# Optimization experiments

Hardware: AMD Instinct MI355X
Metric: run time of the kernel (lower is better)

Reference implementation:

```python
import jax, jax.numpy as jnp
import numpy as np

WS = 7  # window size

def rel_pos_index(ws):
    coords = np.stack(np.meshgrid(np.arange(ws), np.arange(ws), indexing='ij'))  # [2,ws,ws]
    cf = coords.reshape(2, -1)                      # [2, N]
    rel = (cf[:, :, None] - cf[:, None, :]).transpose(1, 2, 0)  # [N,N,2]
    rel[:, :, 0] += ws - 1
    rel[:, :, 1] += ws - 1
    rel[:, :, 0] *= 2 * ws - 1
    return rel.sum(-1)                              # [N,N] int

REL_IDX = rel_pos_index(WS)

def setup_inputs() -> dict:
    key = jax.random.key(0)
    ks = jax.random.split(key, 7)
    B, nW, H, N, D = 32, 64, 6, WS * WS, 32
    C = H * D
    return {
        "x": jax.random.normal(ks[0], (B * nW, N, C), jnp.float32),
        "q_global": jax.random.normal(ks[1], (B, 1, H, N, D), jnp.float32),
        "w_qkv": jax.random.normal(ks[2], (2 * C, C), jnp.float32) * 0.02,
        "b_qkv": jax.random.normal(ks[3], (2 * C,), jnp.float32) * 0.02,
        "bias_table": jax.random.normal(ks[4], ((2 * WS - 1) ** 2, H), jnp.float32) * 0.02,
        "w_proj": jax.random.normal(ks[5], (C, C), jnp.float32) * 0.02,
        "b_proj": jax.random.normal(ks[6], (C,), jnp.float32) * 0.02,
    }

def reference(x, q_global, w_qkv, b_qkv, bias_table, w_proj, b_proj):
    B_, N, C = x.shape
    B, _, H, _, D = q_global.shape
    scale = D ** -0.5
    # K,V projection: [B_, N, 2C] -> two [B_, H, N, D]
    kv = x @ w_qkv.T + b_qkv
    k, v = jnp.split(kv, 2, axis=-1)
    k = k.reshape(B_, N, H, D).transpose(0, 2, 1, 3)
    v = v.reshape(B_, N, H, D).transpose(0, 2, 1, 3)
    # Global query repeated over windows per image
    rep = B_ // B
    q = jnp.broadcast_to(q_global, (B, rep, H, N, D)).reshape(B_, H, N, D) * scale
    attn = jnp.einsum('bhnd,bhmd->bhnm', q, k)  # [B_, H, N, N]
    bias = bias_table[REL_IDX.reshape(-1)].reshape(N, N, H).transpose(2, 0, 1)  # [H,N,N]
    attn = jax.nn.softmax(attn + bias[None], axis=-1)
    out = jnp.einsum('bhnm,bhmd->bhnd', attn, v).transpose(0, 2, 1, 3).reshape(B_, N, C)
    return out @ w_proj.T + b_proj
```

## Files before the change

### kernel.cpp

```cpp
#include <hip/hip_runtime.h>
#include <hip/hip_bf16.h>

typedef __attribute__((ext_vector_type(8))) short short8;
typedef __attribute__((ext_vector_type(4))) short short4v;
typedef __attribute__((ext_vector_type(4))) float f32x4;

#define MFMA16(A,B,C) __builtin_amdgcn_mfma_f32_16x16x32_bf16((A),(B),(C),0,0,0)

static __device__ __forceinline__ unsigned short f2bf(float f) {
  unsigned int u = __float_as_uint(f);
  unsigned int rnd = 0x7fffu + ((u >> 16) & 1u);
  return (unsigned short)((u + rnd) >> 16);
}

__global__ void prep_kernel(const float* __restrict__ qg,
                            const float* __restrict__ wqkv,
                            const float* __restrict__ wproj,
                            const float* __restrict__ btab,
                            unsigned short* __restrict__ wq_c,
                            unsigned short* __restrict__ wp_c,
                            unsigned short* __restrict__ q_bf,
                            float* __restrict__ bias_c)
{
  const int t = blockIdx.x * 256 + threadIdx.x;
  if (t < 32*6*64*32) {
    const int d = t & 31, n = (t >> 5) & 63;
    const int bh = t >> 11;
    const int h = bh % 6, b = bh / 6;
    float v = 0.f;
    if (n < 49) v = qg[((b * 6 + h) * 49 + n) * 32 + d] * 0.17677669529663687f;
    q_bf[t] = f2bf(v);
  }
  if (t < 8*3*6*64*8) {
    const int e = t & 7, l = (t >> 3) & 63;
    const int kb = (t >> 9) % 6, g = (t >> 9) / 6;
    const int ct = g % 3, wv = g / 3;
    const int j = wv * 48 + ct * 16 + (l & 15);
    const int c = kb * 32 + (l >> 4) * 8 + e;
    wq_c[t] = f2bf(wqkv[j * 192 + c]);
  }
  if (t < 2*6*6*64*8) {
    const int e = t & 7, l = (t >> 3) & 63;
    const int kb = (t >> 9) % 6, g = (t >> 9) / 6;
    const int ct = g % 6, cc = g / 6;
    const int cp = cc * 96 + ct * 16 + (l & 15);
    const int c = kb * 32 + (l >> 4) * 8 + e;
    wp_c[t] = f2bf(wproj[cp * 192 + c]);
  }
  if (t < 6*4*64*16) {
    const int i4 = t & 15;
    const int mt = i4 >> 2, r = i4 & 3;
    const int l = (t >> 4) & 63;
    const int nt = (t >> 10) & 3;
    const int h = t >> 12;
    const int m = mt * 16 + (l >> 4) * 4 + r;
    const int n = nt * 16 + (l & 15);
    float v;
    if (m >= 49) v = -1e30f;
    else if (n >= 49) v = 0.f;
    else {
      const int ci = n / 7, cj = n % 7, mi = m / 7, mj = m % 7;
      const int idx = (ci - mi + 6) * 13 + (cj - mj + 6);
      v = btab[idx * 6 + h];
    }
    bias_c[t] = v;
  }
}

__global__ __launch_bounds__(512, 4)
void fused_win_attn(const float* __restrict__ x,
                    const float* __restrict__ b_qkv,
                    const float* __restrict__ b_proj,
                    const unsigned short* __restrict__ wq_c,
                    const unsigned short* __restrict__ wp_c,
                    const unsigned short* __restrict__ q_bf,
                    const float* __restrict__ bias_c,
                    float* __restrict__ out)
{
  extern __shared__ unsigned short lds[];
  unsigned short* x_lds  = lds;
  unsigned short* k_lds  = lds + 12800;
  unsigned short* vT_lds = lds + 26624;
  unsigned short* o_lds  = lds + 12800;

  const f32x4 ZERO4 = {0.f, 0.f, 0.f, 0.f};
  const int tid = threadIdx.x;
  const int wv = tid >> 6;
  const int l  = tid & 63;
  const int lr = l & 15;
  const int lq = l >> 4;
  const int w  = blockIdx.x;

  {
    const float* xw = x + (size_t)w * (49 * 192);
    for (int i = tid; i < 2352; i += 512) {
      const float4 v = *reinterpret_cast<const float4*>(xw + i * 4);
      const int e = i * 4;
      const int row = e / 192, col = e % 192;
      short4v pk;
      pk[0] = (short)f2bf(v.x); pk[1] = (short)f2bf(v.y);
      pk[2] = (short)f2bf(v.z); pk[3] = (short)f2bf(v.w);
      *reinterpret_cast<short4v*>(&x_lds[row * 200 + col]) = pk;
    }
    for (int i = tid; i < 720; i += 512) {
      const int e = i * 4;
      const int row = 49 + e / 192, col = e % 192;
      short4v z = {0, 0, 0, 0};
      *reinterpret_cast<short4v*>(&x_lds[row * 200 + col]) = z;
    }
  }
  __syncthreads();

  {
    short8 afr[4][6];
#pragma unroll
    for (int mt = 0; mt < 4; ++mt)
#pragma unroll
      for (int kb = 0; kb < 6; ++kb)
        afr[mt][kb] = *reinterpret_cast<const short8*>(
            &x_lds[(mt * 16 + lr) * 200 + kb * 32 + lq * 8]);

    for (int ct = 0; ct < 3; ++ct) {
      const int j = wv * 48 + ct * 16 + lr;
      short8 bfr[6];
#pragma unroll
      for (int kb = 0; kb < 6; ++kb)
        bfr[kb] = *reinterpret_cast<const short8*>(
            &wq_c[((((wv * 3) + ct) * 6 + kb) * 64 + l) * 8]);
      const float bq = b_qkv[j];
      f32x4 acc[4];
#pragma unroll
      for (int mt = 0; mt < 4; ++mt) acc[mt] = ZERO4;
#pragma unroll
      for (int kb = 0; kb < 6; ++kb)
#pragma unroll
        for (int mt = 0; mt < 4; ++mt)
          acc[mt] = MFMA16(afr[mt][kb], bfr[kb], acc[mt]);

      if (j < 192) {
        const int h = j >> 5, d = j & 31;
#pragma unroll
        for (int mt = 0; mt < 4; ++mt) {
          const int n0 = mt * 16 + lq * 4;
#pragma unroll
          for (int r = 0; r < 4; ++r)
            k_lds[h * 2304 + (n0 + r) * 36 + d] = f2bf(acc[mt][r] + bq);
        }
      } else {
        const int jj = j - 192, h = jj >> 5, d = jj & 31;
#pragma unroll
        for (int mt = 0; mt < 4; ++mt) {
          const int n0 = mt * 16 + lq * 4;
          short4v pk;
#pragma unroll
          for (int r = 0; r < 4; ++r) pk[r] = (short)f2bf(acc[mt][r] + bq);
          *reinterpret_cast<short4v*>(&vT_lds[h * 2176 + d * 68 + n0]) = pk;
        }
      }
    }
  }
  __syncthreads();

  unsigned short* p_lds = x_lds + wv * (16 * 72);
  const int nt = wv & 3;
  const int img = w >> 6;
  f32x4 o_reg[3][2];
#pragma unroll
  for (int rd = 0; rd < 3; ++rd) {
    const int h = (wv >> 2) + 2 * rd;
    const short8 aq = *reinterpret_cast<const short8*>(
        &q_bf[((img * 6 + h) * 64 + nt * 16 + lr) * 32 + lq * 8]);
    f32x4 s[4];
#pragma unroll
    for (int mt = 0; mt < 4; ++mt) {
      const unsigned short* kp = &k_lds[h * 2304 + (mt * 16 + lr) * 36 + lq * 8];
      const short4v k0 = *reinterpret_cast<const short4v*>(kp);
      const short4v k1 = *reinterpret_cast<const short4v*>(kp + 4);
      short8 bk;
      bk[0]=k0[0]; bk[1]=k0[1]; bk[2]=k0[2]; bk[3]=k0[3];
      bk[4]=k1[0]; bk[5]=k1[1]; bk[6]=k1[2]; bk[7]=k1[3];
      s[mt] = MFMA16(bk, aq, ZERO4);
    }
    const float* bc = bias_c + ((h * 4 + nt) * 64 + l) * 16;
    float lsum = 0.f;
#pragma unroll
    for (int mt = 0; mt < 4; ++mt) {
      const float4 b4 = *reinterpret_cast<const float4*>(bc + mt * 4);
      const float p0 = __expf(s[mt][0] + b4.x);
      const float p1 = __expf(s[mt][1] + b4.y);
      const float p2 = __expf(s[mt][2] + b4.z);
      const float p3 = __expf(s[mt][3] + b4.w);
      lsum += (p0 + p1) + (p2 + p3);
      short4v pk;
      pk[0] = (short)f2bf(p0); pk[1] = (short)f2bf(p1);
      pk[2] = (short)f2bf(p2); pk[3] = (short)f2bf(p3);
      *reinterpret_cast<short4v*>(&p_lds[lr * 72 + mt * 16 + lq * 4]) = pk;
    }
    lsum += __shfl_xor(lsum, 16, 64);
    lsum += __shfl_xor(lsum, 32, 64);
    const float rs = 1.0f / lsum;
    float rinv[4];
#pragma unroll
    for (int r = 0; r < 4; ++r)
      rinv[r] = __shfl(rs, lq * 4 + r, 16);
    f32x4 o0 = ZERO4, o1 = ZERO4;
#pragma unroll
    for (int kb = 0; kb < 2; ++kb) {
      const short8 pa = *reinterpret_cast<const short8*>(&p_lds[lr * 72 + kb * 32 + lq * 8]);
      const unsigned short* vp0 = &vT_lds[h * 2176 + lr * 68 + kb * 32 + lq * 8];
      const unsigned short* vp1 = &vT_lds[h * 2176 + (16 + lr) * 68 + kb * 32 + lq * 8];
      const short4v a0 = *reinterpret_cast<const short4v*>(vp0);
      const short4v a1 = *reinterpret_cast<const short4v*>(vp0 + 4);
      short8 bv0; bv0[0]=a0[0];bv0[1]=a0[1];bv0[2]=a0[2];bv0[3]=a0[3];
                  bv0[4]=a1[0];bv0[5]=a1[1];bv0[6]=a1[2];bv0[7]=a1[3];
      o0 = MFMA16(pa, bv0, o0);
      const short4v c0 = *reinterpret_cast<const short4v*>(vp1);
      const short4v c1 = *reinterpret_cast<const short4v*>(vp1 + 4);
      short8 bv1; bv1[0]=c0[0];bv1[1]=c0[1];bv1[2]=c0[2];bv1[3]=c0[3];
                  bv1[4]=c1[0];bv1[5]=c1[1];bv1[6]=c1[2];bv1[7]=c1[3];
      o1 = MFMA16(pa, bv1, o1);
    }
#pragma unroll
    for (int r = 0; r < 4; ++r) {
      o_reg[rd][0][r] = o0[r] * rinv[r];
      o_reg[rd][1][r] = o1[r] * rinv[r];
    }
  }
  __syncthreads();

#pragma unroll
  for (int rd = 0; rd < 3; ++rd) {
    const int h = (wv >> 2) + 2 * rd;
#pragma unroll
    for (int r = 0; r < 4; ++r) {
      const int n = nt * 16 + lq * 4 + r;
      o_lds[n * 200 + h * 32 + lr]      = f2bf(o_reg[rd][0][r]);
      o_lds[n * 200 + h * 32 + 16 + lr] = f2bf(o_reg[rd][1][r]);
    }
  }
  __syncthreads();

  {
    const int mt = wv & 3;
    const int cc = wv >> 2;
    short8 af[6];
#pragma unroll
    for (int kb = 0; kb < 6; ++kb)
      af[kb] = *reinterpret_cast<const short8*>(&o_lds[(mt * 16 + lr) * 200 + kb * 32 + lq * 8]);
    float* op = out + (size_t)w * 9408;
    for (int ct = 0; ct < 6; ++ct) {
      const int cp = cc * 96 + ct * 16 + lr;
      short8 bf[6];
#pragma unroll
      for (int kb = 0; kb < 6; ++kb)
        bf[kb] = *reinterpret_cast<const short8*>(
            &wp_c[(((cc * 6 + ct) * 6 + kb) * 64 + l) * 8]);
      f32x4 acc = ZERO4;
#pragma unroll
      for (int kb = 0; kb < 6; ++kb) acc = MFMA16(af[kb], bf[kb], acc);
      const float bb = b_proj[cp];
      const int n0 = mt * 16 + lq * 4;
#pragma unroll
      for (int r = 0; r < 4; ++r)
        if (n0 + r < 49) op[(n0 + r) * 192 + cp] = acc[r] + bb;
    }
  }
}

extern "C" void kernel_launch(void* const* d_in, const int* in_sizes, int n_in,
                              void* d_out, int out_size, void* d_ws, size_t ws_size,
                              hipStream_t stream) {
  const float* x     = (const float*)d_in[0];
  const float* qg    = (const float*)d_in[1];
  const float* wqkv  = (const float*)d_in[2];
  const float* bqkv  = (const float*)d_in[3];
  const float* btab  = (const float*)d_in[4];
  const float* wproj = (const float*)d_in[5];
  const float* bproj = (const float*)d_in[6];
  float* out = (float*)d_out;

  char* ws = (char*)d_ws;
  unsigned short* wq_c  = (unsigned short*)(ws);
  unsigned short* wp_c  = (unsigned short*)(ws + 147456);
  unsigned short* q_bf  = (unsigned short*)(ws + 221184);
  float* bias_c         = (float*)(ws + 1007616);

  hipLaunchKernelGGL(prep_kernel, dim3(1536), dim3(256), 0, stream,
                     qg, wqkv, wproj, btab, wq_c, wp_c, q_bf, bias_c);
  hipLaunchKernelGGL(fused_win_attn, dim3(2048), dim3(512), 79360, stream,
                     x, bqkv, bproj, wq_c, wp_c, q_bf, bias_c, out);
}
```

Measured before the change: 91.58 us.

## Swizzle K/V LDS layout, normalize probabilities before PV, use builtin bf16 convert

Replaces the padded K and V^T shared-memory layouts with unpadded XOR-swizzled layouts. This allows single 16-byte short8 loads instead of paired 8-byte loads, avoids bank conflicts, and shrinks the LDS allocation. Softmax normalization moves before the bf16 packing of P, which removes the per-row shuffles and the output rescale. The hand-written float-to-bf16 rounding is swapped for the library intrinsic.

```diff
diff --git a/kernel.cpp b/kernel.cpp
--- a/kernel.cpp
+++ b/kernel.cpp
@@ -8,9 +8,7 @@
 #define MFMA16(A,B,C) __builtin_amdgcn_mfma_f32_16x16x32_bf16((A),(B),(C),0,0,0)
 
 static __device__ __forceinline__ unsigned short f2bf(float f) {
-  unsigned int u = __float_as_uint(f);
-  unsigned int rnd = 0x7fffu + ((u >> 16) & 1u);
-  return (unsigned short)((u + rnd) >> 16);
+  return __builtin_bit_cast(unsigned short, __float2bfloat16(f));
 }
 
 __global__ void prep_kernel(const float* __restrict__ qg,
@@ -80,7 +78,7 @@
   extern __shared__ unsigned short lds[];
   unsigned short* x_lds  = lds;
   unsigned short* k_lds  = lds + 12800;
-  unsigned short* vT_lds = lds + 26624;
+  unsigned short* vT_lds = lds + 25088;
   unsigned short* o_lds  = lds + 12800;
 
   const f32x4 ZERO4 = {0.f, 0.f, 0.f, 0.f};
@@ -143,8 +141,10 @@
         for (int mt = 0; mt < 4; ++mt) {
           const int n0 = mt * 16 + lq * 4;
 #pragma unroll
-          for (int r = 0; r < 4; ++r)
-            k_lds[h * 2304 + (n0 + r) * 36 + d] = f2bf(acc[mt][r] + bq);
+          for (int r = 0; r < 4; ++r) {
+            const int n = n0 + r;
+            k_lds[h * 2048 + ((n * 32 + d) ^ ((n & 7) << 3))] = f2bf(acc[mt][r] + bq);
+          }
         }
       } else {
         const int jj = j - 192, h = jj >> 5, d = jj & 31;
@@ -154,14 +154,15 @@
           short4v pk;
 #pragma unroll
           for (int r = 0; r < 4; ++r) pk[r] = (short)f2bf(acc[mt][r] + bq);
-          *reinterpret_cast<short4v*>(&vT_lds[h * 2176 + d * 68 + n0]) = pk;
+          *reinterpret_cast<short4v*>(
+              &vT_lds[h * 2048 + ((d * 64 + n0) ^ ((d & 7) << 3))]) = pk;
         }
       }
     }
   }
   __syncthreads();
 
-  unsigned short* p_lds = x_lds + wv * (16 * 72);
+  unsigned short* p_lds = x_lds + wv * 1152;
   const int nt = wv & 3;
   const int img = w >> 6;
   f32x4 o_reg[3][2];
@@ -173,58 +174,45 @@
     f32x4 s[4];
 #pragma unroll
     for (int mt = 0; mt < 4; ++mt) {
-      const unsigned short* kp = &k_lds[h * 2304 + (mt * 16 + lr) * 36 + lq * 8];
-      const short4v k0 = *reinterpret_cast<const short4v*>(kp);
-      const short4v k1 = *reinterpret_cast<const short4v*>(kp + 4);
-      short8 bk;
-      bk[0]=k0[0]; bk[1]=k0[1]; bk[2]=k0[2]; bk[3]=k0[3];
-      bk[4]=k1[0]; bk[5]=k1[1]; bk[6]=k1[2]; bk[7]=k1[3];
+      const short8 bk = *reinterpret_cast<const short8*>(
+          &k_lds[h * 2048 + (((mt * 16 + lr) * 32 + lq * 8) ^ ((lr & 7) << 3))]);
       s[mt] = MFMA16(bk, aq, ZERO4);
     }
     const float* bc = bias_c + ((h * 4 + nt) * 64 + l) * 16;
+    float pv4[4][4];
     float lsum = 0.f;
 #pragma unroll
     for (int mt = 0; mt < 4; ++mt) {
       const float4 b4 = *reinterpret_cast<const float4*>(bc + mt * 4);
-      const float p0 = __expf(s[mt][0] + b4.x);
-      const float p1 = __expf(s[mt][1] + b4.y);
-      const float p2 = __expf(s[mt][2] + b4.z);
-      const float p3 = __expf(s[mt][3] + b4.w);
-      lsum += (p0 + p1) + (p2 + p3);
-      short4v pk;
-      pk[0] = (short)f2bf(p0); pk[1] = (short)f2bf(p1);
-      pk[2] = (short)f2bf(p2); pk[3] = (short)f2bf(p3);
-      *reinterpret_cast<short4v*>(&p_lds[lr * 72 + mt * 16 + lq * 4]) = pk;
+      pv4[mt][0] = __expf(s[mt][0] + b4.x);
+      pv4[mt][1] = __expf(s[mt][1] + b4.y);
+      pv4[mt][2] = __expf(s[mt][2] + b4.z);
+      pv4[mt][3] = __expf(s[mt][3] + b4.w);
+      lsum += (pv4[mt][0] + pv4[mt][1]) + (pv4[mt][2] + pv4[mt][3]);
     }
     lsum += __shfl_xor(lsum, 16, 64);
     lsum += __shfl_xor(lsum, 32, 64);
     const float rs = 1.0f / lsum;
-    float rinv[4];
-#pragma unroll
-    for (int r = 0; r < 4; ++r)
-      rinv[r] = __shfl(rs, lq * 4 + r, 16);
+#pragma unroll
+    for (int mt = 0; mt < 4; ++mt) {
+      short4v pk;
+#pragma unroll
+      for (int r = 0; r < 4; ++r) pk[r] = (short)f2bf(pv4[mt][r] * rs);
+      *reinterpret_cast<short4v*>(&p_lds[lr * 72 + mt * 16 + lq * 4]) = pk;
+    }
     f32x4 o0 = ZERO4, o1 = ZERO4;
 #pragma unroll
     for (int kb = 0; kb < 2; ++kb) {
       const short8 pa = *reinterpret_cast<const short8*>(&p_lds[lr * 72 + kb * 32 + lq * 8]);
-      const unsigned short* vp0 = &vT_lds[h * 2176 + lr * 68 + kb * 32 + lq * 8];
-      const unsigned short* vp1 = &vT_lds[h * 2176 + (16 + lr) * 68 + kb * 32 + lq * 8];
-      const short4v a0 = *reinterpret_cast<const short4v*>(vp0);
-      const short4v a1 = *reinterpret_cast<const short4v*>(vp0 + 4);
-      short8 bv0; bv0[0]=a0[0];bv0[1]=a0[1];bv0[2]=a0[2];bv0[3]=a0[3];
-                  bv0[4]=a1[0];bv0[5]=a1[1];bv0[6]=a1[2];bv0[7]=a1[3];
+      const short8 bv0 = *reinterpret_cast<const short8*>(
+          &vT_lds[h * 2048 + ((lr * 64 + kb * 32 + lq * 8) ^ ((lr & 7) << 3))]);
+      const short8 bv1 = *reinterpret_cast<const short8*>(
+          &vT_lds[h * 2048 + (((16 + lr) * 64 + kb * 32 + lq * 8) ^ ((lr & 7) << 3))]);
       o0 = MFMA16(pa, bv0, o0);
-      const short4v c0 = *reinterpret_cast<const short4v*>(vp1);
-      const short4v c1 = *reinterpret_cast<const short4v*>(vp1 + 4);
-      short8 bv1; bv1[0]=c0[0];bv1[1]=c0[1];bv1[2]=c0[2];bv1[3]=c0[3];
-                  bv1[4]=c1[0];bv1[5]=c1[1];bv1[6]=c1[2];bv1[7]=c1[3];
       o1 = MFMA16(pa, bv1, o1);
     }
-#pragma unroll
-    for (int r = 0; r < 4; ++r) {
-      o_reg[rd][0][r] = o0[r] * rinv[r];
-      o_reg[rd][1][r] = o1[r] * rinv[r];
-    }
+    o_reg[rd][0] = o0;
+    o_reg[rd][1] = o1;
   }
   __syncthreads();
 
@@ -287,6 +275,6 @@
 
   hipLaunchKernelGGL(prep_kernel, dim3(1536), dim3(256), 0, stream,
                      qg, wqkv, wproj, btab, wq_c, wp_c, q_bf, bias_c);
-  hipLaunchKernelGGL(fused_win_attn, dim3(2048), dim3(512), 79360, stream,
+  hipLaunchKernelGGL(fused_win_attn, dim3(2048), dim3(512), 74752, stream,
                      x, bqkv, bproj, wq_c, wp_c, q_bf, bias_c, out);
 }
```

New measurement: 118.0 us. 28.8% more time.
